# Optimization experiments

Measured on AMD Instinct MI355X. Metric: run time of the kernel, lower is better.

The kernel has to match this reference:

```python
import jax, jax.numpy as jnp
import numpy as np

N_NODES = 10000
N_EDGES = 640000
NODE_DIM = 128
EDGE_DIM = 32
OUT_DIM = 128


def setup_inputs() -> dict:
    key = jax.random.key(0)
    k_h, k_e, k_ef, k_w1, k_w2 = jax.random.split(key, 5)
    h = jax.random.normal(k_h, (N_NODES, NODE_DIM), dtype=jnp.float32)
    edge_index = jax.random.randint(k_e, (2, N_EDGES), 0, N_NODES, dtype=jnp.int64)
    edge_features = jax.random.normal(k_ef, (N_EDGES, EDGE_DIM), dtype=jnp.float32)
    in_dim = 2 * NODE_DIM + EDGE_DIM
    # Kaiming-ish init scale for realism
    W1 = jax.random.normal(k_w1, (in_dim, OUT_DIM), dtype=jnp.float32) / np.sqrt(in_dim)
    b1 = jnp.zeros((OUT_DIM,), dtype=jnp.float32)
    W2 = jax.random.normal(k_w2, (OUT_DIM, OUT_DIM), dtype=jnp.float32) / np.sqrt(OUT_DIM)
    b2 = jnp.zeros((OUT_DIM,), dtype=jnp.float32)
    return {"h": h, "edge_index": edge_index, "edge_features": edge_features,
            "n": N_NODES, "W1": W1, "b1": b1, "W2": W2, "b2": b2}


def reference(h, edge_index, edge_features, n, W1, b1, W2, b2):
    rows, cols = edge_index[0], edge_index[1]
    # gather source/target node features + edge features -> [E, 2*node_dim+edge_dim]
    msg_input = jnp.concatenate([h[rows], h[cols], edge_features], axis=-1)
    hidden = jax.nn.relu(msg_input @ W1 + b1)   # [E, out_dim]
    messages = hidden @ W2 + b2                 # [E, out_dim]
    # scatter-add messages onto destination rows -> [n, out_dim]
    out = jax.ops.segment_sum(messages, rows, num_segments=n)
    return out
```

## Files before the change

### kernel.cpp

```cpp
#include <hip/hip_runtime.h>
#include <hip/hip_bf16.h>


typedef __attribute__((ext_vector_type(8))) short bf16x8;
typedef __attribute__((ext_vector_type(4))) short s16x4;
typedef __attribute__((ext_vector_type(4))) float f32x4;

#define ND 128
#define ED 32

__device__ __forceinline__ short f2bf(float x) {
  unsigned int u = __float_as_uint(x);
  unsigned int r = (u + 0x7FFFu + ((u >> 16) & 1u)) >> 16;
  return (short)r;
}

__device__ __forceinline__ float bf2f(short s) {
  return __uint_as_float(((unsigned int)(unsigned short)s) << 16);
}

__device__ __forceinline__ f32x4 bf8lo(bf16x8 v) {
  f32x4 r;
  #pragma unroll
  for (int j = 0; j < 4; ++j) r[j] = bf2f(v[j]);
  return r;
}
__device__ __forceinline__ f32x4 bf8hi(bf16x8 v) {
  f32x4 r;
  #pragma unroll
  for (int j = 0; j < 4; ++j) r[j] = bf2f(v[4 + j]);
  return r;
}

__device__ __forceinline__ int load_idx(const void* ei, long long i, int is64) {
  return is64 ? (int)((const long long*)ei)[i] : ((const int*)ei)[i];
}

__device__ __forceinline__ int detect64(const void* ei) {
  const unsigned int* u = (const unsigned int*)ei;
  int is64 = 1;
  #pragma unroll
  for (int i = 0; i < 16; ++i)
    if (u[2 * i + 1] != 0u) is64 = 0;
  return is64;
}

__device__ __forceinline__ int swz(int c) {
  int ct = c >> 4, li = c & 15;
  return (ct >> 2) * 64 + (li >> 2) * 16 + (ct & 3) * 4 + (li & 3);
}

__global__ __launch_bounds__(256) void prep_hist_kernel(
    const float* __restrict__ W1, const float* __restrict__ W2,
    const void* __restrict__ ei, int* __restrict__ counts,
    int* __restrict__ rank, short* __restrict__ w12t,
    short* __restrict__ w1eA, short* __restrict__ w2t, int E) {
  int b = blockIdx.x;
  if (b < 128) {
    int t = b * 256 + threadIdx.x;
    if (t < 256 * 128) {
      int np = t >> 7, k = t & 127;
      float v = (np < 128) ? W1[k * 128 + np] : W1[(128 + k) * 128 + (np - 128)];
      w12t[t] = f2bf(v);
    }
    if (t < 128 * 128) {
      int n = t >> 7, k = t & 127;
      w2t[t] = f2bf(W2[k * 128 + n]);
    }
    if (t < 8 * 64 * 8) {
      int ct = t >> 9, lane = (t >> 3) & 63, j = t & 7;
      int li = lane & 15, lg = lane >> 4;
      w1eA[t] = f2bf(W1[(256 + lg * 8 + j) * 128 + ct * 16 + li]);
    }
  } else {
    int e = (b - 128) * 256 + threadIdx.x;
    if (e < E) {
      int is64 = detect64(ei);
      int r = load_idx(ei, e, is64);
      rank[e] = atomicAdd(&counts[r], 1);
    }
  }
}

__global__ __launch_bounds__(1024) void scan_kernel(const int* __restrict__ counts,
                                                    int* __restrict__ row_ptr, int n) {
  __shared__ int wtot[16];
  int tid = threadIdx.x;
  int lane = tid & 63, w = tid >> 6;
  int base_i = tid * 16;
  int c[16];
  int tot = 0;
  #pragma unroll
  for (int j = 0; j < 16; ++j) {
    int i = base_i + j;
    c[j] = (i < n) ? counts[i] : 0;
    tot += c[j];
  }
  int x = tot;
  #pragma unroll
  for (int d = 1; d < 64; d <<= 1) {
    int t = __shfl_up(x, d);
    if (lane >= d) x += t;
  }
  if (lane == 63) wtot[w] = x;
  __syncthreads();
  if (w == 0) {
    int y = (lane < 16) ? wtot[lane] : 0;
    #pragma unroll
    for (int d = 1; d < 16; d <<= 1) {
      int t = __shfl_up(y, d);
      if (lane >= d) y += t;
    }
    if (lane < 16) wtot[lane] = y;
  }
  __syncthreads();
  int waveoff = (w == 0) ? 0 : wtot[w - 1];
  int run = waveoff + x - tot;
  if (tid == 0) row_ptr[0] = 0;
  #pragma unroll
  for (int j = 0; j < 16; ++j) {
    int i = base_i + j;
    if (i < n) {
      run += c[j];
      row_ptr[i + 1] = run;
    }
  }
}

template <int MODE>
__global__ __launch_bounds__(256, 4) void scatter_sg_kernel(
    const void* __restrict__ ei, const float* __restrict__ ef,
    const int* __restrict__ row_ptr, const int* __restrict__ rank,
    const float* __restrict__ h, const short* __restrict__ w12t,
    const float* __restrict__ b1, short* __restrict__ efb,
    int* __restrict__ ccol, int2* __restrict__ ec,
    float* __restrict__ s2, short* __restrict__ g2, int N, int E) {
  int b = blockIdx.x;
  int SGB = (N + 63) >> 6;
  if (b < SGB) {
    int lane = threadIdx.x & 63, w = threadIdx.x >> 6;
    int li = lane & 15, lg = lane >> 4;
    int base = b * 64 + w * 16;
    int rowm = base + li;
    if (rowm >= N) rowm = N - 1;
    float breg[8];
    #pragma unroll
    for (int nt = 0; nt < 8; ++nt) breg[nt] = b1[nt * 16 + li];
    f32x4 acc[16];
    #pragma unroll
    for (int nt = 0; nt < 16; ++nt) acc[nt] = (f32x4){0.f, 0.f, 0.f, 0.f};
    #pragma unroll
    for (int kc = 0; kc < 4; ++kc) {
      f32x4 f0 = *(const f32x4*)(h + (size_t)rowm * ND + kc * 32 + lg * 8);
      f32x4 f1 = *(const f32x4*)(h + (size_t)rowm * ND + kc * 32 + lg * 8 + 4);
      bf16x8 a;
      #pragma unroll
      for (int j = 0; j < 4; ++j) { a[j] = f2bf(f0[j]); a[4 + j] = f2bf(f1[j]); }
      #pragma unroll
      for (int nt = 0; nt < 16; ++nt) {
        bf16x8 bb = *(const bf16x8*)(w12t + (nt * 16 + li) * 128 + kc * 32 + lg * 8);
        acc[nt] = __builtin_amdgcn_mfma_f32_16x16x32_bf16(a, bb, acc[nt], 0, 0, 0);
      }
    }
    #pragma unroll
    for (int nt = 0; nt < 16; ++nt)
      #pragma unroll
      for (int r = 0; r < 4; ++r) {
        int row = base + lg * 4 + r;
        if (row < N) {
          if (nt < 8) {
            int o = swz(nt * 16 + li);
            s2[(size_t)row * 128 + o] = acc[nt][r] + breg[nt];
          } else {
            int o = swz((nt - 8) * 16 + li);
            g2[(size_t)row * 128 + o] = f2bf(acc[nt][r]);
          }
        }
      }
  } else {
    int gt = (b - SGB) * 256 + threadIdx.x;
    int e = gt >> 2, part = gt & 3;
    if (e < E) {
      int is64 = detect64(ei);
      int r = load_idx(ei, e, is64);
      int c = load_idx(ei, (long long)E + e, is64);
      int pos = row_ptr[r] + rank[e];
      if (MODE == 0) {
        f32x4 a0 = *(const f32x4*)(ef + (size_t)e * ED + part * 8);
        f32x4 a1 = *(const f32x4*)(ef + (size_t)e * ED + part * 8 + 4);
        bf16x8 ob;
        #pragma unroll
        for (int j = 0; j < 4; ++j) { ob[j] = f2bf(a0[j]); ob[4 + j] = f2bf(a1[j]); }
        *(bf16x8*)(efb + (size_t)pos * ED + part * 8) = ob;
        if (part == 0) ccol[pos] = c;
      } else {
        if (part == 0) ec[pos] = make_int2(e, c);
      }
    }
  }
}

template <int MODE>
__global__ __launch_bounds__(128, 4) void layer1_kernel(
    const float* __restrict__ s2, const short* __restrict__ g2,
    const short* __restrict__ efb, const float* __restrict__ ef,
    const int* __restrict__ ccol, const int2* __restrict__ ec,
    const short* __restrict__ w1eA, const int* __restrict__ row_ptr,
    float* __restrict__ hsum) {
  int node = blockIdx.x;
  int lane = threadIdx.x & 63;
  int w = threadIdx.x >> 6;
  int li = lane & 15, lg = lane >> 4;
  int rp = row_ptr[node], rpe = row_ptr[node + 1];
  int deg = rpe - rp;

  if (deg == 0) {
    if (li == 0) {
      #pragma unroll
      for (int nt = 0; nt < 4; ++nt)
        *(f32x4*)(hsum + (size_t)node * 128 + (w * 4 + nt) * 16 + lg * 4) =
            (f32x4){0.f, 0.f, 0.f, 0.f};
    }
    return;
  }

  bf16x8 wa[4];
  #pragma unroll
  for (int nt = 0; nt < 4; ++nt)
    wa[nt] = *(const bf16x8*)(w1eA + ((w * 4 + nt) * 64 + lane) * 8);
  f32x4 sreg[4];
  #pragma unroll
  for (int nt = 0; nt < 4; ++nt)
    sreg[nt] = *(const f32x4*)(s2 + (size_t)node * 128 + w * 64 + lg * 16 + nt * 4);
  f32x4 psum[4];
  #pragma unroll
  for (int nt = 0; nt < 4; ++nt) psum[nt] = (f32x4){0.f, 0.f, 0.f, 0.f};

  int ntiles = (deg + 15) >> 4;
  int last = rpe - 1;
  auto ppos = [&](int t) {
    int p = rp + t * 16 + li;
    return p > last ? last : p;
  };

  if (MODE == 0) {
    int p0 = ppos(0), p1 = ppos(1);
    int c0 = ccol[p0], c1 = ccol[p1];
    bf16x8 bf0 = *(const bf16x8*)(efb + (size_t)p0 * ED + lg * 8);
    bf16x8 bf1 = *(const bf16x8*)(efb + (size_t)p1 * ED + lg * 8);
    bf16x8 ga = *(const bf16x8*)(g2 + (size_t)c0 * 128 + w * 64 + lg * 16);
    bf16x8 gb = *(const bf16x8*)(g2 + (size_t)c0 * 128 + w * 64 + lg * 16 + 8);
    for (int t = 0; t < ntiles; ++t) {
      int p2 = ppos(t + 2);
      int c2 = ccol[p2];
      bf16x8 bf2 = *(const bf16x8*)(efb + (size_t)p2 * ED + lg * 8);
      bf16x8 gan = *(const bf16x8*)(g2 + (size_t)c1 * 128 + w * 64 + lg * 16);
      bf16x8 gbn = *(const bf16x8*)(g2 + (size_t)c1 * 128 + w * 64 + lg * 16 + 8);
      f32x4 a0 = __builtin_amdgcn_mfma_f32_16x16x32_bf16(wa[0], bf0, (f32x4){0.f,0.f,0.f,0.f}, 0, 0, 0);
      f32x4 a1 = __builtin_amdgcn_mfma_f32_16x16x32_bf16(wa[1], bf0, (f32x4){0.f,0.f,0.f,0.f}, 0, 0, 0);
      f32x4 a2 = __builtin_amdgcn_mfma_f32_16x16x32_bf16(wa[2], bf0, (f32x4){0.f,0.f,0.f,0.f}, 0, 0, 0);
      f32x4 a3 = __builtin_amdgcn_mfma_f32_16x16x32_bf16(wa[3], bf0, (f32x4){0.f,0.f,0.f,0.f}, 0, 0, 0);
      if ((t * 16 + li) < deg) {
        f32x4 v0 = a0 + sreg[0] + bf8lo(ga);
        f32x4 v1 = a1 + sreg[1] + bf8hi(ga);
        f32x4 v2 = a2 + sreg[2] + bf8lo(gb);
        f32x4 v3 = a3 + sreg[3] + bf8hi(gb);
        #pragma unroll
        for (int r = 0; r < 4; ++r) {
          psum[0][r] += (v0[r] > 0.f ? v0[r] : 0.f);
          psum[1][r] += (v1[r] > 0.f ? v1[r] : 0.f);
          psum[2][r] += (v2[r] > 0.f ? v2[r] : 0.f);
          psum[3][r] += (v3[r] > 0.f ? v3[r] : 0.f);
        }
      }
      c0 = c1; c1 = c2; bf0 = bf1; bf1 = bf2; ga = gan; gb = gbn;
    }
  } else {
    int2 i0 = ec[ppos(0)], i1 = ec[ppos(1)];
    f32x4 e0 = *(const f32x4*)(ef + (size_t)i0.x * ED + lg * 8);
    f32x4 e1 = *(const f32x4*)(ef + (size_t)i0.x * ED + lg * 8 + 4);
    bf16x8 ga = *(const bf16x8*)(g2 + (size_t)i0.y * 128 + w * 64 + lg * 16);
    bf16x8 gb = *(const bf16x8*)(g2 + (size_t)i0.y * 128 + w * 64 + lg * 16 + 8);
    for (int t = 0; t < ntiles; ++t) {
      int2 i2 = ec[ppos(t + 2)];
      f32x4 e0n = *(const f32x4*)(ef + (size_t)i1.x * ED + lg * 8);
      f32x4 e1n = *(const f32x4*)(ef + (size_t)i1.x * ED + lg * 8 + 4);
      bf16x8 gan = *(const bf16x8*)(g2 + (size_t)i1.y * 128 + w * 64 + lg * 16);
      bf16x8 gbn = *(const bf16x8*)(g2 + (size_t)i1.y * 128 + w * 64 + lg * 16 + 8);
      bf16x8 bf;
      #pragma unroll
      for (int j = 0; j < 4; ++j) { bf[j] = f2bf(e0[j]); bf[4 + j] = f2bf(e1[j]); }
      f32x4 a0 = __builtin_amdgcn_mfma_f32_16x16x32_bf16(wa[0], bf, (f32x4){0.f,0.f,0.f,0.f}, 0, 0, 0);
      f32x4 a1 = __builtin_amdgcn_mfma_f32_16x16x32_bf16(wa[1], bf, (f32x4){0.f,0.f,0.f,0.f}, 0, 0, 0);
      f32x4 a2 = __builtin_amdgcn_mfma_f32_16x16x32_bf16(wa[2], bf, (f32x4){0.f,0.f,0.f,0.f}, 0, 0, 0);
      f32x4 a3 = __builtin_amdgcn_mfma_f32_16x16x32_bf16(wa[3], bf, (f32x4){0.f,0.f,0.f,0.f}, 0, 0, 0);
      if ((t * 16 + li) < deg) {
        f32x4 v0 = a0 + sreg[0] + bf8lo(ga);
        f32x4 v1 = a1 + sreg[1] + bf8hi(ga);
        f32x4 v2 = a2 + sreg[2] + bf8lo(gb);
        f32x4 v3 = a3 + sreg[3] + bf8hi(gb);
        #pragma unroll
        for (int r = 0; r < 4; ++r) {
          psum[0][r] += (v0[r] > 0.f ? v0[r] : 0.f);
          psum[1][r] += (v1[r] > 0.f ? v1[r] : 0.f);
          psum[2][r] += (v2[r] > 0.f ? v2[r] : 0.f);
          psum[3][r] += (v3[r] > 0.f ? v3[r] : 0.f);
        }
      }
      i0 = i1; i1 = i2; e0 = e0n; e1 = e1n; ga = gan; gb = gbn;
    }
  }

  #pragma unroll
  for (int nt = 0; nt < 4; ++nt)
    #pragma unroll
    for (int r = 0; r < 4; ++r) {
      float v = psum[nt][r];
      v += __shfl_xor(v, 1);
      v += __shfl_xor(v, 2);
      v += __shfl_xor(v, 4);
      v += __shfl_xor(v, 8);
      psum[nt][r] = v;
    }
  if (li == 0) {
    #pragma unroll
    for (int nt = 0; nt < 4; ++nt)
      *(f32x4*)(hsum + (size_t)node * 128 + (w * 4 + nt) * 16 + lg * 4) = psum[nt];
  }
}

__global__ __launch_bounds__(256) void out_kernel(const float* __restrict__ hsum,
                                                  const short* __restrict__ w2t,
                                                  const float* __restrict__ b2,
                                                  const int* __restrict__ row_ptr,
                                                  float* __restrict__ out, int N) {
  int lane = threadIdx.x & 63, w = threadIdx.x >> 6;
  int li = lane & 15, lg = lane >> 4;
  int base = blockIdx.x * 64 + w * 16;
  int rowm = base + li;
  if (rowm >= N) rowm = N - 1;
  float breg[8];
  #pragma unroll
  for (int nt = 0; nt < 8; ++nt) breg[nt] = b2[nt * 16 + li];
  f32x4 acc[8];
  #pragma unroll
  for (int nt = 0; nt < 8; ++nt) acc[nt] = (f32x4){0.f, 0.f, 0.f, 0.f};
  #pragma unroll
  for (int kc = 0; kc < 4; ++kc) {
    f32x4 f0 = *(const f32x4*)(hsum + (size_t)rowm * 128 + kc * 32 + lg * 8);
    f32x4 f1 = *(const f32x4*)(hsum + (size_t)rowm * 128 + kc * 32 + lg * 8 + 4);
    bf16x8 a;
    #pragma unroll
    for (int j = 0; j < 4; ++j) { a[j] = f2bf(f0[j]); a[4 + j] = f2bf(f1[j]); }
    #pragma unroll
    for (int nt = 0; nt < 8; ++nt) {
      bf16x8 bb = *(const bf16x8*)(w2t + (nt * 16 + li) * 128 + kc * 32 + lg * 8);
      acc[nt] = __builtin_amdgcn_mfma_f32_16x16x32_bf16(a, bb, acc[nt], 0, 0, 0);
    }
  }
  #pragma unroll
  for (int r = 0; r < 4; ++r) {
    int row = base + lg * 4 + r;
    if (row < N) {
      float dg = (float)(row_ptr[row + 1] - row_ptr[row]);
      #pragma unroll
      for (int nt = 0; nt < 8; ++nt)
        out[(size_t)row * 128 + nt * 16 + li] = acc[nt][r] + dg * breg[nt];
    }
  }
}

extern "C" void kernel_launch(void* const* d_in, const int* in_sizes, int n_in,
                              void* d_out, int out_size, void* d_ws, size_t ws_size,
                              hipStream_t stream) {
  const float* h  = (const float*)d_in[0];
  const void*  ei = d_in[1];
  const float* ef = (const float*)d_in[2];
  const float* W1 = (const float*)d_in[4];
  const float* b1 = (const float*)d_in[5];
  const float* W2 = (const float*)d_in[6];
  const float* b2 = (const float*)d_in[7];
  float* out = (float*)d_out;
  int N = in_sizes[0] / ND;
  int E = in_sizes[2] / ED;

  char* ws = (char*)d_ws;
  size_t off = 0;
  auto alloc = [&](size_t bytes) {
    size_t o = off;
    off = (off + bytes + 255) & ~(size_t)255;
    return o;
  };
  int*   counts  = (int*)(ws + alloc((size_t)N * 4));
  int*   row_ptr = (int*)(ws + alloc((size_t)(N + 1) * 4));
  int*   rank    = (int*)(ws + alloc((size_t)E * 4));
  short* w12t    = (short*)(ws + alloc(256 * 128 * 2));
  short* w1eA    = (short*)(ws + alloc(8 * 64 * 8 * 2));
  short* w2t     = (short*)(ws + alloc(128 * 128 * 2));
  float* s2      = (float*)(ws + alloc((size_t)N * 128 * 4));
  short* g2      = (short*)(ws + alloc((size_t)N * 128 * 2));
  float* hsumb   = (float*)(ws + alloc((size_t)N * 128 * 4));
  size_t branch_off = off;
  short* efb  = (short*)(ws + branch_off);
  int*   ccol = (int*)(ws + ((branch_off + (size_t)E * ED * 2 + 255) & ~(size_t)255));
  size_t need0 = ((branch_off + (size_t)E * ED * 2 + 255) & ~(size_t)255) + (size_t)E * 4;
  int2* ec = (int2*)(ws + branch_off);
  size_t need1 = branch_off + (size_t)E * 8;
  int mode = (ws_size >= need0) ? 0 : 1;
  (void)need1;

  int SGB = (N + 63) >> 6;
  int SCB = (4 * E + 255) / 256;

  hipMemsetAsync(counts, 0, (size_t)N * 4, stream);
  prep_hist_kernel<<<128 + (E + 255) / 256, 256, 0, stream>>>(
      W1, W2, ei, counts, rank, w12t, w1eA, w2t, E);
  scan_kernel<<<1, 1024, 0, stream>>>(counts, row_ptr, N);
  if (mode == 0) {
    scatter_sg_kernel<0><<<SGB + SCB, 256, 0, stream>>>(
        ei, ef, row_ptr, rank, h, w12t, b1, efb, ccol, ec, s2, g2, N, E);
    layer1_kernel<0><<<N, 128, 0, stream>>>(s2, g2, efb, ef, ccol, ec, w1eA, row_ptr, hsumb);
  } else {
    scatter_sg_kernel<1><<<SGB + SCB, 256, 0, stream>>>(
        ei, ef, row_ptr, rank, h, w12t, b1, efb, ccol, ec, s2, g2, N, E);
    layer1_kernel<1><<<N, 128, 0, stream>>>(s2, g2, efb, ef, ccol, ec, w1eA, row_ptr, hsumb);
  }
  out_kernel<<<(N + 63) / 64, 256, 0, stream>>>(hsumb, w2t, b2, row_ptr, out, N);
}
```

Before: 134.5 us.

## Drop bf16 edge-feature staging and split edge tiles across waves in layer1

The scatter pass no longer converts and reorders edge features into a sorted bf16 buffer. It only writes (edge id, col) pairs, and layer1 gathers fp32 edge features directly by edge id and converts them in-kernel. Layer1 now has each wave take alternate 16-edge tiles across all 128 output columns, with a shared-memory reduction between the two waves, instead of splitting the columns between waves. This removes the staged write and read of edge features and halves MFMA redundancy per edge, at the cost of random fp32 gathers and more registers per wave.

```diff
diff --git a/kernel.cpp b/kernel.cpp
--- a/kernel.cpp
+++ b/kernel.cpp
@@ -3,7 +3,6 @@
 
 
 typedef __attribute__((ext_vector_type(8))) short bf16x8;
-typedef __attribute__((ext_vector_type(4))) short s16x4;
 typedef __attribute__((ext_vector_type(4))) float f32x4;
 
 #define ND 128
@@ -46,8 +45,8 @@
 }
 
 __device__ __forceinline__ int swz(int c) {
-  int ct = c >> 4, li = c & 15;
-  return (ct >> 2) * 64 + (li >> 2) * 16 + (ct & 3) * 4 + (li & 3);
+  int ct = c >> 4, cc = c & 15;
+  return (ct >> 2) * 64 + (cc >> 2) * 16 + (ct & 3) * 4 + (cc & 3);
 }
 
 __global__ __launch_bounds__(256) void prep_hist_kernel(
@@ -127,14 +126,12 @@
   }
 }
 
-template <int MODE>
 __global__ __launch_bounds__(256, 4) void scatter_sg_kernel(
-    const void* __restrict__ ei, const float* __restrict__ ef,
-    const int* __restrict__ row_ptr, const int* __restrict__ rank,
-    const float* __restrict__ h, const short* __restrict__ w12t,
-    const float* __restrict__ b1, short* __restrict__ efb,
-    int* __restrict__ ccol, int2* __restrict__ ec,
-    float* __restrict__ s2, short* __restrict__ g2, int N, int E) {
+    const void* __restrict__ ei, const int* __restrict__ row_ptr,
+    const int* __restrict__ rank, const float* __restrict__ h,
+    const short* __restrict__ w12t, const float* __restrict__ b1,
+    int2* __restrict__ ec, float* __restrict__ s2, short* __restrict__ g2,
+    int N, int E) {
   int b = blockIdx.x;
   int SGB = (N + 63) >> 6;
   if (b < SGB) {
@@ -169,42 +166,26 @@
         int row = base + lg * 4 + r;
         if (row < N) {
           if (nt < 8) {
-            int o = swz(nt * 16 + li);
-            s2[(size_t)row * 128 + o] = acc[nt][r] + breg[nt];
+            s2[(size_t)row * 128 + swz(nt * 16 + li)] = acc[nt][r] + breg[nt];
           } else {
-            int o = swz((nt - 8) * 16 + li);
-            g2[(size_t)row * 128 + o] = f2bf(acc[nt][r]);
+            g2[(size_t)row * 128 + swz((nt - 8) * 16 + li)] = f2bf(acc[nt][r]);
           }
         }
       }
   } else {
-    int gt = (b - SGB) * 256 + threadIdx.x;
-    int e = gt >> 2, part = gt & 3;
+    int e = (b - SGB) * 256 + threadIdx.x;
     if (e < E) {
       int is64 = detect64(ei);
       int r = load_idx(ei, e, is64);
       int c = load_idx(ei, (long long)E + e, is64);
-      int pos = row_ptr[r] + rank[e];
-      if (MODE == 0) {
-        f32x4 a0 = *(const f32x4*)(ef + (size_t)e * ED + part * 8);
-        f32x4 a1 = *(const f32x4*)(ef + (size_t)e * ED + part * 8 + 4);
-        bf16x8 ob;
-        #pragma unroll
-        for (int j = 0; j < 4; ++j) { ob[j] = f2bf(a0[j]); ob[4 + j] = f2bf(a1[j]); }
-        *(bf16x8*)(efb + (size_t)pos * ED + part * 8) = ob;
-        if (part == 0) ccol[pos] = c;
-      } else {
-        if (part == 0) ec[pos] = make_int2(e, c);
-      }
-    }
-  }
-}
-
-template <int MODE>
-__global__ __launch_bounds__(128, 4) void layer1_kernel(
+      ec[row_ptr[r] + rank[e]] = make_int2(e, c);
+    }
+  }
+}
+
+__global__ __launch_bounds__(128) void layer1_kernel(
     const float* __restrict__ s2, const short* __restrict__ g2,
-    const short* __restrict__ efb, const float* __restrict__ ef,
-    const int* __restrict__ ccol, const int2* __restrict__ ec,
+    const float* __restrict__ ef, const int2* __restrict__ ec,
     const short* __restrict__ w1eA, const int* __restrict__ row_ptr,
     float* __restrict__ hsum) {
   int node = blockIdx.x;
@@ -213,119 +194,96 @@
   int li = lane & 15, lg = lane >> 4;
   int rp = row_ptr[node], rpe = row_ptr[node + 1];
   int deg = rpe - rp;
-
-  if (deg == 0) {
-    if (li == 0) {
-      #pragma unroll
-      for (int nt = 0; nt < 4; ++nt)
-        *(f32x4*)(hsum + (size_t)node * 128 + (w * 4 + nt) * 16 + lg * 4) =
-            (f32x4){0.f, 0.f, 0.f, 0.f};
-    }
-    return;
-  }
-
-  bf16x8 wa[4];
-  #pragma unroll
-  for (int nt = 0; nt < 4; ++nt)
-    wa[nt] = *(const bf16x8*)(w1eA + ((w * 4 + nt) * 64 + lane) * 8);
-  f32x4 sreg[4];
-  #pragma unroll
-  for (int nt = 0; nt < 4; ++nt)
-    sreg[nt] = *(const f32x4*)(s2 + (size_t)node * 128 + w * 64 + lg * 16 + nt * 4);
-  f32x4 psum[4];
-  #pragma unroll
-  for (int nt = 0; nt < 4; ++nt) psum[nt] = (f32x4){0.f, 0.f, 0.f, 0.f};
-
-  int ntiles = (deg + 15) >> 4;
-  int last = rpe - 1;
-  auto ppos = [&](int t) {
-    int p = rp + t * 16 + li;
-    return p > last ? last : p;
-  };
-
-  if (MODE == 0) {
-    int p0 = ppos(0), p1 = ppos(1);
-    int c0 = ccol[p0], c1 = ccol[p1];
-    bf16x8 bf0 = *(const bf16x8*)(efb + (size_t)p0 * ED + lg * 8);
-    bf16x8 bf1 = *(const bf16x8*)(efb + (size_t)p1 * ED + lg * 8);
-    bf16x8 ga = *(const bf16x8*)(g2 + (size_t)c0 * 128 + w * 64 + lg * 16);
-    bf16x8 gb = *(const bf16x8*)(g2 + (size_t)c0 * 128 + w * 64 + lg * 16 + 8);
-    for (int t = 0; t < ntiles; ++t) {
-      int p2 = ppos(t + 2);
-      int c2 = ccol[p2];
-      bf16x8 bf2 = *(const bf16x8*)(efb + (size_t)p2 * ED + lg * 8);
-      bf16x8 gan = *(const bf16x8*)(g2 + (size_t)c1 * 128 + w * 64 + lg * 16);
-      bf16x8 gbn = *(const bf16x8*)(g2 + (size_t)c1 * 128 + w * 64 + lg * 16 + 8);
-      f32x4 a0 = __builtin_amdgcn_mfma_f32_16x16x32_bf16(wa[0], bf0, (f32x4){0.f,0.f,0.f,0.f}, 0, 0, 0);
-      f32x4 a1 = __builtin_amdgcn_mfma_f32_16x16x32_bf16(wa[1], bf0, (f32x4){0.f,0.f,0.f,0.f}, 0, 0, 0);
-      f32x4 a2 = __builtin_amdgcn_mfma_f32_16x16x32_bf16(wa[2], bf0, (f32x4){0.f,0.f,0.f,0.f}, 0, 0, 0);
-      f32x4 a3 = __builtin_amdgcn_mfma_f32_16x16x32_bf16(wa[3], bf0, (f32x4){0.f,0.f,0.f,0.f}, 0, 0, 0);
+  __shared__ float red[128];
+
+  f32x4 psum[8];
+  #pragma unroll
+  for (int ct = 0; ct < 8; ++ct) psum[ct] = (f32x4){0.f, 0.f, 0.f, 0.f};
+
+  if (deg > 0) {
+    bf16x8 wa[8];
+    #pragma unroll
+    for (int ct = 0; ct < 8; ++ct)
+      wa[ct] = *(const bf16x8*)(w1eA + ((ct * 64 + lane) * 8));
+    f32x4 sreg[8];
+    #pragma unroll
+    for (int ct = 0; ct < 8; ++ct)
+      sreg[ct] = *(const f32x4*)(s2 + (size_t)node * 128 + (ct >> 2) * 64 + lg * 16 + (ct & 3) * 4);
+
+    int ntiles = (deg + 15) >> 4;
+    int last = rpe - 1;
+    auto ppos = [&](int t) {
+      int p = rp + t * 16 + li;
+      return p > last ? last : p;
+    };
+
+    int2 iA = ec[ppos(w)];
+    int2 iB = ec[ppos(w + 2)];
+    f32x4 eA0 = *(const f32x4*)(ef + (size_t)iA.x * ED + lg * 8);
+    f32x4 eA1 = *(const f32x4*)(ef + (size_t)iA.x * ED + lg * 8 + 4);
+    const short* gpA = g2 + (size_t)iA.y * 128;
+    bf16x8 gA00 = *(const bf16x8*)(gpA + lg * 16);
+    bf16x8 gA01 = *(const bf16x8*)(gpA + lg * 16 + 8);
+    bf16x8 gA10 = *(const bf16x8*)(gpA + 64 + lg * 16);
+    bf16x8 gA11 = *(const bf16x8*)(gpA + 64 + lg * 16 + 8);
+
+    for (int t = w; t < ntiles; t += 2) {
+      int2 iC = ec[ppos(t + 4)];
+      f32x4 eB0 = *(const f32x4*)(ef + (size_t)iB.x * ED + lg * 8);
+      f32x4 eB1 = *(const f32x4*)(ef + (size_t)iB.x * ED + lg * 8 + 4);
+      const short* gpB = g2 + (size_t)iB.y * 128;
+      bf16x8 gB00 = *(const bf16x8*)(gpB + lg * 16);
+      bf16x8 gB01 = *(const bf16x8*)(gpB + lg * 16 + 8);
+      bf16x8 gB10 = *(const bf16x8*)(gpB + 64 + lg * 16);
+      bf16x8 gB11 = *(const bf16x8*)(gpB + 64 + lg * 16 + 8);
+      bf16x8 bfrag;
+      #pragma unroll
+      for (int j = 0; j < 4; ++j) { bfrag[j] = f2bf(eA0[j]); bfrag[4 + j] = f2bf(eA1[j]); }
+      f32x4 acc[8];
+      #pragma unroll
+      for (int ct = 0; ct < 8; ++ct)
+        acc[ct] = __builtin_amdgcn_mfma_f32_16x16x32_bf16(wa[ct], bfrag,
+                                                          (f32x4){0.f, 0.f, 0.f, 0.f}, 0, 0, 0);
       if ((t * 16 + li) < deg) {
-        f32x4 v0 = a0 + sreg[0] + bf8lo(ga);
-        f32x4 v1 = a1 + sreg[1] + bf8hi(ga);
-        f32x4 v2 = a2 + sreg[2] + bf8lo(gb);
-        f32x4 v3 = a3 + sreg[3] + bf8hi(gb);
         #pragma unroll
-        for (int r = 0; r < 4; ++r) {
-          psum[0][r] += (v0[r] > 0.f ? v0[r] : 0.f);
-          psum[1][r] += (v1[r] > 0.f ? v1[r] : 0.f);
-          psum[2][r] += (v2[r] > 0.f ? v2[r] : 0.f);
-          psum[3][r] += (v3[r] > 0.f ? v3[r] : 0.f);
+        for (int ct = 0; ct < 8; ++ct) {
+          bf16x8 gr = (ct < 4) ? ((ct & 2) ? gA01 : gA00) : ((ct & 2) ? gA11 : gA10);
+          f32x4 gv = (ct & 1) ? bf8hi(gr) : bf8lo(gr);
+          f32x4 v = acc[ct] + sreg[ct] + gv;
+          #pragma unroll
+          for (int r = 0; r < 4; ++r)
+            psum[ct][r] += (v[r] > 0.f ? v[r] : 0.f);
         }
       }
-      c0 = c1; c1 = c2; bf0 = bf1; bf1 = bf2; ga = gan; gb = gbn;
-    }
-  } else {
-    int2 i0 = ec[ppos(0)], i1 = ec[ppos(1)];
-    f32x4 e0 = *(const f32x4*)(ef + (size_t)i0.x * ED + lg * 8);
-    f32x4 e1 = *(const f32x4*)(ef + (size_t)i0.x * ED + lg * 8 + 4);
-    bf16x8 ga = *(const bf16x8*)(g2 + (size_t)i0.y * 128 + w * 64 + lg * 16);
-    bf16x8 gb = *(const bf16x8*)(g2 + (size_t)i0.y * 128 + w * 64 + lg * 16 + 8);
-    for (int t = 0; t < ntiles; ++t) {
-      int2 i2 = ec[ppos(t + 2)];
-      f32x4 e0n = *(const f32x4*)(ef + (size_t)i1.x * ED + lg * 8);
-      f32x4 e1n = *(const f32x4*)(ef + (size_t)i1.x * ED + lg * 8 + 4);
-      bf16x8 gan = *(const bf16x8*)(g2 + (size_t)i1.y * 128 + w * 64 + lg * 16);
-      bf16x8 gbn = *(const bf16x8*)(g2 + (size_t)i1.y * 128 + w * 64 + lg * 16 + 8);
-      bf16x8 bf;
-      #pragma unroll
-      for (int j = 0; j < 4; ++j) { bf[j] = f2bf(e0[j]); bf[4 + j] = f2bf(e1[j]); }
-      f32x4 a0 = __builtin_amdgcn_mfma_f32_16x16x32_bf16(wa[0], bf, (f32x4){0.f,0.f,0.f,0.f}, 0, 0, 0);
-      f32x4 a1 = __builtin_amdgcn_mfma_f32_16x16x32_bf16(wa[1], bf, (f32x4){0.f,0.f,0.f,0.f}, 0, 0, 0);
-      f32x4 a2 = __builtin_amdgcn_mfma_f32_16x16x32_bf16(wa[2], bf, (f32x4){0.f,0.f,0.f,0.f}, 0, 0, 0);
-      f32x4 a3 = __builtin_amdgcn_mfma_f32_16x16x32_bf16(wa[3], bf, (f32x4){0.f,0.f,0.f,0.f}, 0, 0, 0);
-      if ((t * 16 + li) < deg) {
-        f32x4 v0 = a0 + sreg[0] + bf8lo(ga);
-        f32x4 v1 = a1 + sreg[1] + bf8hi(ga);
-        f32x4 v2 = a2 + sreg[2] + bf8lo(gb);
-        f32x4 v3 = a3 + sreg[3] + bf8hi(gb);
-        #pragma unroll
-        for (int r = 0; r < 4; ++r) {
-          psum[0][r] += (v0[r] > 0.f ? v0[r] : 0.f);
-          psum[1][r] += (v1[r] > 0.f ? v1[r] : 0.f);
-          psum[2][r] += (v2[r] > 0.f ? v2[r] : 0.f);
-          psum[3][r] += (v3[r] > 0.f ? v3[r] : 0.f);
-        }
-      }
-      i0 = i1; i1 = i2; e0 = e0n; e1 = e1n; ga = gan; gb = gbn;
-    }
-  }
-
-  #pragma unroll
-  for (int nt = 0; nt < 4; ++nt)
+      iA = iB; iB = iC;
+      eA0 = eB0; eA1 = eB1;
+      gA00 = gB00; gA01 = gB01; gA10 = gB10; gA11 = gB11;
+    }
+  }
+
+  #pragma unroll
+  for (int ct = 0; ct < 8; ++ct)
     #pragma unroll
     for (int r = 0; r < 4; ++r) {
-      float v = psum[nt][r];
+      float v = psum[ct][r];
       v += __shfl_xor(v, 1);
       v += __shfl_xor(v, 2);
       v += __shfl_xor(v, 4);
       v += __shfl_xor(v, 8);
-      psum[nt][r] = v;
-    }
-  if (li == 0) {
-    #pragma unroll
-    for (int nt = 0; nt < 4; ++nt)
-      *(f32x4*)(hsum + (size_t)node * 128 + (w * 4 + nt) * 16 + lg * 4) = psum[nt];
+      psum[ct][r] = v;
+    }
+  if (w == 1 && li == 0) {
+    #pragma unroll
+    for (int ct = 0; ct < 8; ++ct)
+      *(f32x4*)(red + ct * 16 + lg * 4) = psum[ct];
+  }
+  __syncthreads();
+  if (w == 0 && li == 0) {
+    #pragma unroll
+    for (int ct = 0; ct < 8; ++ct) {
+      f32x4 o = psum[ct] + *(const f32x4*)(red + ct * 16 + lg * 4);
+      *(f32x4*)(hsum + (size_t)node * 128 + ct * 16 + lg * 4) = o;
+    }
   }
 }
 
@@ -373,9 +331,9 @@
 extern "C" void kernel_launch(void* const* d_in, const int* in_sizes, int n_in,
                               void* d_out, int out_size, void* d_ws, size_t ws_size,
                               hipStream_t stream) {
-  const float* h  = (const float*)d_in[0];
   const void*  ei = d_in[1];
   const float* ef = (const float*)d_in[2];
+  const float* h  = (const float*)d_in[0];
   const float* W1 = (const float*)d_in[4];
   const float* b1 = (const float*)d_in[5];
   const float* W2 = (const float*)d_in[6];
@@ -400,30 +358,17 @@
   float* s2      = (float*)(ws + alloc((size_t)N * 128 * 4));
   short* g2      = (short*)(ws + alloc((size_t)N * 128 * 2));
   float* hsumb   = (float*)(ws + alloc((size_t)N * 128 * 4));
-  size_t branch_off = off;
-  short* efb  = (short*)(ws + branch_off);
-  int*   ccol = (int*)(ws + ((branch_off + (size_t)E * ED * 2 + 255) & ~(size_t)255));
-  size_t need0 = ((branch_off + (size_t)E * ED * 2 + 255) & ~(size_t)255) + (size_t)E * 4;
-  int2* ec = (int2*)(ws + branch_off);
-  size_t need1 = branch_off + (size_t)E * 8;
-  int mode = (ws_size >= need0) ? 0 : 1;
-  (void)need1;
+  int2*  ec      = (int2*)(ws + alloc((size_t)E * 8));
 
   int SGB = (N + 63) >> 6;
-  int SCB = (4 * E + 255) / 256;
+  int SCB = (E + 255) / 256;
 
   hipMemsetAsync(counts, 0, (size_t)N * 4, stream);
   prep_hist_kernel<<<128 + (E + 255) / 256, 256, 0, stream>>>(
       W1, W2, ei, counts, rank, w12t, w1eA, w2t, E);
   scan_kernel<<<1, 1024, 0, stream>>>(counts, row_ptr, N);
-  if (mode == 0) {
-    scatter_sg_kernel<0><<<SGB + SCB, 256, 0, stream>>>(
-        ei, ef, row_ptr, rank, h, w12t, b1, efb, ccol, ec, s2, g2, N, E);
-    layer1_kernel<0><<<N, 128, 0, stream>>>(s2, g2, efb, ef, ccol, ec, w1eA, row_ptr, hsumb);
-  } else {
-    scatter_sg_kernel<1><<<SGB + SCB, 256, 0, stream>>>(
-        ei, ef, row_ptr, rank, h, w12t, b1, efb, ccol, ec, s2, g2, N, E);
-    layer1_kernel<1><<<N, 128, 0, stream>>>(s2, g2, efb, ef, ccol, ec, w1eA, row_ptr, hsumb);
-  }
+  scatter_sg_kernel<<<SGB + SCB, 256, 0, stream>>>(
+      ei, row_ptr, rank, h, w12t, b1, ec, s2, g2, N, E);
+  layer1_kernel<<<N, 128, 0, stream>>>(s2, g2, ef, ec, w1eA, row_ptr, hsumb);
   out_kernel<<<(N + 63) / 64, 256, 0, stream>>>(hsumb, w2t, b2, row_ptr, out, N);
 }
```

After: 142.0 us. +5.6%, slower.
